# Kernel tuning notes

Hardware: AMD Instinct MI355X
Metric: run time of the kernel (lower is better)

## Reference

```python
import jax, jax.numpy as jnp
import numpy as np

N = 50000      # nodes
E = 400000     # edges
F_IN = 64      # raw node feat
E_IN = 16      # raw edge feat
H = 128        # hidden
L = 4          # PNAConv layers
G = 256        # graphs in batch
OUT = 12       # classes
EPS = 1e-5


def setup_inputs() -> dict:
    key = jax.random.key(0)
    ks = jax.random.split(key, 24)
    s = 0.05
    inp = {
        'x': jax.random.normal(ks[0], (N, F_IN), jnp.float32),
        'edge_attr': jax.random.normal(ks[1], (E, E_IN), jnp.float32),
        'src': jax.random.randint(ks[2], (E,), 0, N, jnp.int32),
        'dst': jax.random.randint(ks[3], (E,), 0, N, jnp.int32),
        'batch': jnp.sort(jax.random.randint(ks[4], (N,), 0, G, jnp.int32)),
        'node_emb_W': jax.random.normal(ks[5], (F_IN, H), jnp.float32) * s,
        'node_emb_b': jnp.zeros((H,), jnp.float32),
        'edge_emb_W': jax.random.normal(ks[6], (E_IN, H), jnp.float32) * s,
        'edge_emb_b': jnp.zeros((H,), jnp.float32),
        'edge_enc_W': jax.random.normal(ks[7], (L, H, H), jnp.float32) * s,
        'edge_enc_b': jnp.zeros((L, H), jnp.float32),
        'pre_W': jax.random.normal(ks[8], (L, 3 * H, H), jnp.float32) * s,
        'pre_b': jnp.zeros((L, H), jnp.float32),
        'post_W': jax.random.normal(ks[9], (L, 13 * H, H), jnp.float32) * s,
        'post_b': jnp.zeros((L, H), jnp.float32),
        'lin_W': jax.random.normal(ks[10], (L, H, H), jnp.float32) * s,
        'lin_b': jnp.zeros((L, H), jnp.float32),
        'head_W': jax.random.normal(ks[11], (H, OUT), jnp.float32) * s,
        'head_b': jnp.zeros((OUT,), jnp.float32),
    }
    return inp


def pna_forward(x, edge_attr, src, dst, batch,
                node_emb_W, node_emb_b, edge_emb_W, edge_emb_b,
                edge_enc_W, edge_enc_b, pre_W, pre_b,
                post_W, post_b, lin_W, lin_b, head_W, head_b):
    n = x.shape[0]
    h = x @ node_emb_W + node_emb_b                     # [N,H]
    e0 = edge_attr @ edge_emb_W + edge_emb_b           # [E,H]

    ones = jnp.ones((src.shape[0],), jnp.float32)
    deg = jax.ops.segment_sum(ones, dst, num_segments=n)        # in-degree
    degc = jnp.maximum(deg, 1.0)                                 # PyG clamp_(1)
    avg_log = jnp.mean(jnp.log1p(deg))                           # avg_deg['log'] from histogram
    amp = (jnp.log(degc + 1.0) / avg_log)[:, None]               # amplification scaler
    att = (avg_log / jnp.log(degc + 1.0))[:, None]               # attenuation scaler
    has_nbr = (deg > 0)[:, None]

    for l in range(L):
        e = e0 @ edge_enc_W[l] + edge_enc_b[l]                   # [E,H]
        W = pre_W[l]
        # pre_nn(cat(x_i, x_j, e)) without materializing the 3H concat
        m = (jnp.take(h, dst, axis=0) @ W[:H] +
             jnp.take(h, src, axis=0) @ W[H:2 * H] +
             e @ W[2 * H:] + pre_b[l])                           # [E,H]
        s1 = jax.ops.segment_sum(m, dst, num_segments=n)
        mean = s1 / degc[:, None]
        mean2 = jax.ops.segment_sum(m * m, dst, num_segments=n) / degc[:, None]
        std = jnp.sqrt(jax.nn.relu(mean2 - mean * mean) + EPS)
        mn = jnp.where(has_nbr, jax.ops.segment_min(m, dst, num_segments=n), 0.0)
        mx = jnp.where(has_nbr, jax.ops.segment_max(m, dst, num_segments=n), 0.0)
        agg = jnp.concatenate([mean, mn, mx, std], axis=-1)      # [N,4H]
        scaled = jnp.concatenate([agg, agg * amp, agg * att], axis=-1)  # [N,12H]
        out = jnp.concatenate([h, scaled], axis=-1) @ post_W[l] + post_b[l]
        h = jax.nn.relu(out @ lin_W[l] + lin_b[l])               # dropout = identity (eval)

    g = jax.ops.segment_sum(h, batch, num_segments=G)            # global_add_pool
    return g @ head_W + head_b                                   # [G,12]


def reference(x, edge_attr, src, dst, batch,
              node_emb_W, node_emb_b, edge_emb_W, edge_emb_b,
              edge_enc_W, edge_enc_b, pre_W, pre_b,
              post_W, post_b, lin_W, lin_b, head_W, head_b):
    return pna_forward(x, edge_attr, src, dst, batch,
                       node_emb_W, node_emb_b, edge_emb_W, edge_emb_b,
                       edge_enc_W, edge_enc_b, pre_W, pre_b,
                       post_W, post_b, lin_W, lin_b, head_W, head_b)
```

## Files before the change

### kernel.cpp

```cpp
#include <hip/hip_runtime.h>

#define NN 50000
#define NE 400000
#define FIN 64
#define EIN 16
#define H 128
#define NL 4
#define NG 256
#define NOUT 12
#define EPSV 1e-5f

#define SB 256
#define NBLK ((NN + SB - 1) / SB)
#define GB2 ((NN + 127) / 128)
#define NP64 (NN * 64)

typedef short bf16x8 __attribute__((ext_vector_type(8)));
typedef float f32x4 __attribute__((ext_vector_type(4)));
typedef float v2f __attribute__((ext_vector_type(2)));

__device__ __forceinline__ unsigned short f2bf(float f) {
    unsigned u = __float_as_uint(f);
    u += 0x7fffu + ((u >> 16) & 1u);
    return (unsigned short)(u >> 16);
}

__device__ __forceinline__ float bflo(unsigned u) { return __uint_as_float(u << 16); }
__device__ __forceinline__ float bfhi(unsigned u) { return __uint_as_float(u & 0xffff0000u); }

__global__ void k_hist(const int* __restrict__ dst, int* __restrict__ deg) {
    int e = blockIdx.x * 256 + threadIdx.x;
    if (e < NE) atomicAdd(&deg[dst[e]], 1);
}

__global__ void k_scan1(const int* __restrict__ deg, int* __restrict__ partial) {
    __shared__ int sm[256];
    int i = blockIdx.x * 256 + threadIdx.x;
    sm[threadIdx.x] = (i < NN) ? deg[i] : 0;
    __syncthreads();
    for (int s = 128; s > 0; s >>= 1) {
        if (threadIdx.x < s) sm[threadIdx.x] += sm[threadIdx.x + s];
        __syncthreads();
    }
    if (threadIdx.x == 0) partial[blockIdx.x] = sm[0];
}

__global__ void k_scan2(int* __restrict__ partial, int* __restrict__ row_ptr, int nblk) {
    __shared__ int sm[256];
    int t = threadIdx.x;
    sm[t] = (t < nblk) ? partial[t] : 0;
    __syncthreads();
    for (int off = 1; off < 256; off <<= 1) {
        int v = (t >= off) ? sm[t - off] : 0;
        __syncthreads();
        sm[t] += v;
        __syncthreads();
    }
    int excl = (t == 0) ? 0 : sm[t - 1];
    if (t < nblk) partial[t] = excl;
    if (t == 0) row_ptr[0] = 0;
}

__global__ void k_scan3(const int* __restrict__ deg, const int* __restrict__ partial,
                        int* __restrict__ row_ptr) {
    __shared__ int sm[256];
    int t = threadIdx.x;
    int i = blockIdx.x * 256 + t;
    sm[t] = (i < NN) ? deg[i] : 0;
    __syncthreads();
    for (int off = 1; off < 256; off <<= 1) {
        int v = (t >= off) ? sm[t - off] : 0;
        __syncthreads();
        sm[t] += v;
        __syncthreads();
    }
    if (i < NN) row_ptr[i + 1] = partial[blockIdx.x] + sm[t];
}

__global__ void k_fill(const int* __restrict__ src, const int* __restrict__ dst,
                       const int* __restrict__ row_ptr, int* __restrict__ cursor,
                       int* __restrict__ csr_src, int* __restrict__ csr_eid) {
    int e = blockIdx.x * 256 + threadIdx.x;
    if (e >= NE) return;
    int d = dst[e];
    int pos = atomicAdd(&cursor[d], 1);
    int slot = row_ptr[d] + pos;
    csr_src[slot] = src[e];
    csr_eid[slot] = e;
}

__global__ void k_eperm(const float* __restrict__ eattr, const int* __restrict__ csr_eid,
                        float* __restrict__ eattrF) {
    int idx = blockIdx.x * 256 + threadIdx.x;
    if (idx >= NE * EIN) return;
    int slot = idx >> 4, j = idx & 15;
    eattrF[idx] = eattr[(size_t)csr_eid[slot] * EIN + j];
}

__global__ void k_sumlog(const int* __restrict__ deg, float* __restrict__ sum) {
    int i = blockIdx.x * 256 + threadIdx.x;
    float v = (i < NN) ? log1pf((float)deg[i]) : 0.f;
    #pragma unroll
    for (int off = 32; off > 0; off >>= 1) v += __shfl_down(v, off, 64);
    if ((threadIdx.x & 63) == 0) atomicAdd(sum, v);
}

__global__ void k_scalers(const int* __restrict__ deg, const float* __restrict__ sumlog,
                          float* __restrict__ amp, float* __restrict__ att) {
    int i = blockIdx.x * 256 + threadIdx.x;
    if (i >= NN) return;
    float avg = sumlog[0] / (float)NN;
    float degc = fmaxf((float)deg[i], 1.0f);
    float la = logf(degc + 1.0f);
    amp[i] = la / avg;
    att[i] = avg / la;
}

__global__ __launch_bounds__(256) void k_encfold(const float* __restrict__ encW,
                                                 const float* __restrict__ preW,
                                                 float* __restrict__ M) {
    __shared__ float As[32][68];
    __shared__ float Bs[32][128];
    int l = blockIdx.y;
    const float* A = encW + (size_t)l * H * H;
    const float* Bp = preW + (size_t)l * 3 * H * H + 2 * H * H;
    float* Ml = M + (size_t)l * H * H;
    int m0 = blockIdx.x * 64;
    int tid = threadIdx.x;
    int tx = tid & 31, ty = tid >> 5;
    float4 acc[8];
    #pragma unroll
    for (int r = 0; r < 8; r++) acc[r] = make_float4(0, 0, 0, 0);
    int f = tid & 7, r0 = tid >> 3;
    int cf = tid & 31, kr0 = tid >> 5;
    for (int k0 = 0; k0 < H; k0 += 32) {
        #pragma unroll
        for (int hh = 0; hh < 2; hh++) {
            int r = r0 + hh * 32;
            float4 v = *(const float4*)(A + (size_t)(m0 + r) * H + k0 + f * 4);
            As[f * 4 + 0][r] = v.x; As[f * 4 + 1][r] = v.y;
            As[f * 4 + 2][r] = v.z; As[f * 4 + 3][r] = v.w;
        }
        #pragma unroll
        for (int hh = 0; hh < 4; hh++) {
            int kr = kr0 + hh * 8;
            *(float4*)&Bs[kr][cf * 4] = *(const float4*)(Bp + (size_t)(k0 + kr) * H + cf * 4);
        }
        __syncthreads();
        #pragma unroll
        for (int kk = 0; kk < 32; kk++) {
            float4 b = *(float4*)&Bs[kk][tx * 4];
            float4 a0 = *(float4*)&As[kk][ty * 8];
            float4 a1 = *(float4*)&As[kk][ty * 8 + 4];
            acc[0].x = fmaf(a0.x, b.x, acc[0].x); acc[0].y = fmaf(a0.x, b.y, acc[0].y);
            acc[0].z = fmaf(a0.x, b.z, acc[0].z); acc[0].w = fmaf(a0.x, b.w, acc[0].w);
            acc[1].x = fmaf(a0.y, b.x, acc[1].x); acc[1].y = fmaf(a0.y, b.y, acc[1].y);
            acc[1].z = fmaf(a0.y, b.z, acc[1].z); acc[1].w = fmaf(a0.y, b.w, acc[1].w);
            acc[2].x = fmaf(a0.z, b.x, acc[2].x); acc[2].y = fmaf(a0.z, b.y, acc[2].y);
            acc[2].z = fmaf(a0.z, b.z, acc[2].z); acc[2].w = fmaf(a0.z, b.w, acc[2].w);
            acc[3].x = fmaf(a0.w, b.x, acc[3].x); acc[3].y = fmaf(a0.w, b.y, acc[3].y);
            acc[3].z = fmaf(a0.w, b.z, acc[3].z); acc[3].w = fmaf(a0.w, b.w, acc[3].w);
            acc[4].x = fmaf(a1.x, b.x, acc[4].x); acc[4].y = fmaf(a1.x, b.y, acc[4].y);
            acc[4].z = fmaf(a1.x, b.z, acc[4].z); acc[4].w = fmaf(a1.x, b.w, acc[4].w);
            acc[5].x = fmaf(a1.y, b.x, acc[5].x); acc[5].y = fmaf(a1.y, b.y, acc[5].y);
            acc[5].z = fmaf(a1.y, b.z, acc[5].z); acc[5].w = fmaf(a1.y, b.w, acc[5].w);
            acc[6].x = fmaf(a1.z, b.x, acc[6].x); acc[6].y = fmaf(a1.z, b.y, acc[6].y);
            acc[6].z = fmaf(a1.z, b.z, acc[6].z); acc[6].w = fmaf(a1.z, b.w, acc[6].w);
            acc[7].x = fmaf(a1.w, b.x, acc[7].x); acc[7].y = fmaf(a1.w, b.y, acc[7].y);
            acc[7].z = fmaf(a1.w, b.z, acc[7].z); acc[7].w = fmaf(a1.w, b.w, acc[7].w);
        }
        __syncthreads();
    }
    #pragma unroll
    for (int rr = 0; rr < 8; rr++) {
        int row = m0 + ty * 8 + rr;
        *(float4*)(Ml + (size_t)row * H + tx * 4) = acc[rr];
    }
}

__global__ void k_kprep(const float* __restrict__ embW, const float* __restrict__ M,
                        float* __restrict__ Kc) {
    int l = blockIdx.y;
    int idx = blockIdx.x * 256 + threadIdx.x;
    int r = idx >> 7, j = idx & 127;
    const float* Ml = M + (size_t)l * H * H;
    float s = 0.f;
    for (int k = 0; k < H; k++) s = fmaf(embW[r * H + k], Ml[k * H + j], s);
    Kc[l * 16 * H + idx] = s;
}

__global__ void k_cprep(const float* __restrict__ emb_b, const float* __restrict__ encW,
                        const float* __restrict__ enc_b, const float* __restrict__ preW,
                        const float* __restrict__ pre_b, float* __restrict__ cc) {
    __shared__ float b1[H];
    int l = blockIdx.x, t = threadIdx.x;
    const float* encWl = encW + (size_t)l * H * H;
    const float* preW2 = preW + (size_t)l * 3 * H * H + 2 * H * H;
    float s = enc_b[l * H + t];
    for (int k = 0; k < H; k++) s = fmaf(emb_b[k], encWl[k * H + t], s);
    b1[t] = s;
    __syncthreads();
    float c = pre_b[l * H + t];
    for (int k = 0; k < H; k++) c = fmaf(b1[k], preW2[k * H + t], c);
    cc[l * H + t] = c;
}

struct TD { const float* S; unsigned short* D; int K; };
struct TDs { TD t[9]; };

__global__ void k_prepw(TDs p) {
    TD d = p.t[blockIdx.y];
    int idx = blockIdx.x * 256 + threadIdx.x;
    int total = d.K << 7;
    if (idx < total) {
        int k = idx >> 7, n = idx & 127;
        d.D[(size_t)n * d.K + k] = f2bf(d.S[(size_t)k * 128 + n]);
    }
}

__global__ void k_cast(const float* __restrict__ S, unsigned short* __restrict__ D, int n) {
    int i = blockIdx.x * 256 + threadIdx.x;
    if (i < n) D[i] = f2bf(S[i]);
}

__global__ __launch_bounds__(256) void k_wfold(const float* __restrict__ postW,
                                               const float* __restrict__ linW,
                                               unsigned short* __restrict__ Wt3,
                                               unsigned short* __restrict__ foldT) {
    __shared__ float As[32][68];
    __shared__ float Bs[32][128];
    int l = blockIdx.y;
    const float* A = postW + (size_t)l * 13 * H * H;
    const float* Bp = linW + (size_t)l * H * H;
    int m0 = blockIdx.x * 64;
    int tid = threadIdx.x;
    int tx = tid & 31, ty = tid >> 5;
    float4 acc[8];
    #pragma unroll
    for (int r = 0; r < 8; r++) acc[r] = make_float4(0, 0, 0, 0);
    int f = tid & 7, r0 = tid >> 3;
    int cf = tid & 31, kr0 = tid >> 5;
    for (int k0 = 0; k0 < H; k0 += 32) {
        #pragma unroll
        for (int hh = 0; hh < 2; hh++) {
            int r = r0 + hh * 32;
            float4 v = *(const float4*)(A + (size_t)(m0 + r) * H + k0 + f * 4);
            As[f * 4 + 0][r] = v.x; As[f * 4 + 1][r] = v.y;
            As[f * 4 + 2][r] = v.z; As[f * 4 + 3][r] = v.w;
        }
        #pragma unroll
        for (int hh = 0; hh < 4; hh++) {
            int kr = kr0 + hh * 8;
            *(float4*)&Bs[kr][cf * 4] = *(const float4*)(Bp + (size_t)(k0 + kr) * H + cf * 4);
        }
        __syncthreads();
        #pragma unroll
        for (int kk = 0; kk < 32; kk++) {
            float4 b = *(float4*)&Bs[kk][tx * 4];
            float4 a0 = *(float4*)&As[kk][ty * 8];
            float4 a1 = *(float4*)&As[kk][ty * 8 + 4];
            acc[0].x = fmaf(a0.x, b.x, acc[0].x); acc[0].y = fmaf(a0.x, b.y, acc[0].y);
            acc[0].z = fmaf(a0.x, b.z, acc[0].z); acc[0].w = fmaf(a0.x, b.w, acc[0].w);
            acc[1].x = fmaf(a0.y, b.x, acc[1].x); acc[1].y = fmaf(a0.y, b.y, acc[1].y);
            acc[1].z = fmaf(a0.y, b.z, acc[1].z); acc[1].w = fmaf(a0.y, b.w, acc[1].w);
            acc[2].x = fmaf(a0.z, b.x, acc[2].x); acc[2].y = fmaf(a0.z, b.y, acc[2].y);
            acc[2].z = fmaf(a0.z, b.z, acc[2].z); acc[2].w = fmaf(a0.z, b.w, acc[2].w);
            acc[3].x = fmaf(a0.w, b.x, acc[3].x); acc[3].y = fmaf(a0.w, b.y, acc[3].y);
            acc[3].z = fmaf(a0.w, b.z, acc[3].z); acc[3].w = fmaf(a0.w, b.w, acc[3].w);
            acc[4].x = fmaf(a1.x, b.x, acc[4].x); acc[4].y = fmaf(a1.x, b.y, acc[4].y);
            acc[4].z = fmaf(a1.x, b.z, acc[4].z); acc[4].w = fmaf(a1.x, b.w, acc[4].w);
            acc[5].x = fmaf(a1.y, b.x, acc[5].x); acc[5].y = fmaf(a1.y, b.y, acc[5].y);
            acc[5].z = fmaf(a1.y, b.z, acc[5].z); acc[5].w = fmaf(a1.y, b.w, acc[5].w);
            acc[6].x = fmaf(a1.z, b.x, acc[6].x); acc[6].y = fmaf(a1.z, b.y, acc[6].y);
            acc[6].z = fmaf(a1.z, b.z, acc[6].z); acc[6].w = fmaf(a1.z, b.w, acc[6].w);
            acc[7].x = fmaf(a1.w, b.x, acc[7].x); acc[7].y = fmaf(a1.w, b.y, acc[7].y);
            acc[7].z = fmaf(a1.w, b.z, acc[7].z); acc[7].w = fmaf(a1.w, b.w, acc[7].w);
        }
        __syncthreads();
    }
    unsigned short* w2 = Wt3 + (size_t)(l * 3 + 2) * H * H;
    unsigned short* ft = foldT + (size_t)l * 128 * 1664;
    int r = m0 + ty * 8;
    #pragma unroll
    for (int c = 0; c < 4; c++) {
        int n = tx * 4 + c;
        unsigned short tmp[8] __attribute__((aligned(16)));
        #pragma unroll
        for (int rr = 0; rr < 8; rr++) tmp[rr] = f2bf(((const float*)&acc[rr])[c]);
        unsigned short* dstp = (r < 128) ? (w2 + (size_t)n * 128 + r)
                                         : (ft + (size_t)n * 1664 + r);
        *(uint4*)dstp = *(const uint4*)tmp;
    }
}

__global__ void k_bfold(const float* __restrict__ pb, const float* __restrict__ lb,
                        const float* __restrict__ linW, float* __restrict__ cf) {
    int l = blockIdx.x, n = threadIdx.x;
    const float* B = linW + (size_t)l * H * H;
    float s = lb[l * H + n];
    for (int j = 0; j < H; j++) s = fmaf(pb[l * H + j], B[j * H + n], s);
    cf[l * H + n] = s;
}

__global__ __launch_bounds__(256, 4) void k_mgemm(
    const unsigned short* __restrict__ A, int lda, int K, int nch,
    const unsigned short* __restrict__ Bt, int ldb, int bstride_y,
    const float* __restrict__ bias, unsigned short* __restrict__ outB)
{
    __shared__ unsigned short SH[2][128][72];
    const unsigned short* Btp = Bt + (size_t)blockIdx.x * bstride_y;
    int m0 = blockIdx.y * 128;
    int tid = threadIdx.x;
    int wave = tid >> 6, lane = tid & 63;
    int wr = wave >> 1, wc = wave & 1;
    int ln = lane & 15, q = lane >> 4;

    f32x4 acc[4][4];
    #pragma unroll
    for (int a = 0; a < 4; a++)
        #pragma unroll
        for (int b = 0; b < 4; b++) acc[a][b] = (f32x4){0.f, 0.f, 0.f, 0.f};

    for (int c = 0; c < nch; c++) {
        int col = c * 64;
        #pragma unroll
        for (int i0 = 0; i0 < 4; i0++) {
            int i = tid + i0 * 256;
            int row = i >> 3, seg = i & 7;
            uint4 bv = *(const uint4*)(Btp + (size_t)row * ldb + col + seg * 8);
            *(uint4*)(&SH[1][row][seg * 8]) = bv;
            int rowg = m0 + row;
            uint4 av = make_uint4(0, 0, 0, 0);
            if (rowg < NN) av = *(const uint4*)(A + (size_t)rowg * lda + col + seg * 8);
            *(uint4*)(&SH[0][row][seg * 8]) = av;
        }
        __syncthreads();
        #pragma unroll
        for (int kq = 0; kq < 2; kq++) {
            bf16x8 af[4], bfr[4];
            #pragma unroll
            for (int f = 0; f < 4; f++) {
                af[f]  = *(const bf16x8*)(&SH[0][wr * 64 + f * 16 + ln][kq * 32 + q * 8]);
                bfr[f] = *(const bf16x8*)(&SH[1][wc * 64 + f * 16 + ln][kq * 32 + q * 8]);
            }
            #pragma unroll
            for (int fr = 0; fr < 4; fr++)
                #pragma unroll
                for (int fc = 0; fc < 4; fc++)
                    acc[fr][fc] = __builtin_amdgcn_mfma_f32_16x16x32_bf16(
                        bfr[fc], af[fr], acc[fr][fc], 0, 0, 0);
        }
        __syncthreads();
    }

    unsigned short* CT = &SH[0][0][0];
    #pragma unroll
    for (int fr = 0; fr < 4; fr++) {
        int rloc = wr * 64 + fr * 16 + ln;
        #pragma unroll
        for (int fc = 0; fc < 4; fc++) {
            int colb = wc * 64 + fc * 16 + q * 4;
            float4 bv = bias ? *(const float4*)(bias + colb) : make_float4(0, 0, 0, 0);
            unsigned short tmp[4] __attribute__((aligned(8)));
            tmp[0] = f2bf(acc[fr][fc][0] + bv.x);
            tmp[1] = f2bf(acc[fr][fc][1] + bv.y);
            tmp[2] = f2bf(acc[fr][fc][2] + bv.z);
            tmp[3] = f2bf(acc[fr][fc][3] + bv.w);
            *(uint2*)(&CT[rloc * 136 + colb]) = *(const uint2*)tmp;
        }
    }
    __syncthreads();
    unsigned short* outBp = outB + (size_t)blockIdx.x * NN * H;
    #pragma unroll
    for (int i0 = 0; i0 < 8; i0++) {
        int idx = tid + i0 * 256;
        int row = idx >> 4, seg = idx & 15;
        int rowg = m0 + row;
        if (rowg < NN)
            *(uint4*)(outBp + (size_t)rowg * H + seg * 8) = *(const uint4*)(&CT[row * 136 + seg * 8]);
    }
}

__global__ __launch_bounds__(256) void k_agg2(
    const unsigned short* __restrict__ pd, const unsigned short* __restrict__ ps,
    const float* __restrict__ eF,
    const int* __restrict__ csr_src, const int* __restrict__ row_ptr,
    const float* __restrict__ Kl, const float* __restrict__ cl,
    unsigned short* __restrict__ agg)
{
    int wv = threadIdx.x >> 6, lane = threadIdx.x & 63;
    int i = blockIdx.x * 4 + wv;
    int d0 = lane * 2;
    v2f kr[16];
    #pragma unroll
    for (int k = 0; k < 16; k++) kr[k] = *(const v2f*)(Kl + k * H + d0);
    v2f c2 = *(const v2f*)(cl + d0);
    unsigned hd = *(const unsigned*)(pd + (size_t)i * H + d0);
    v2f base = c2 + (v2f){bflo(hd), bfhi(hd)};
    int rs = __builtin_amdgcn_readfirstlane(row_ptr[i]);
    int re = __builtin_amdgcn_readfirstlane(row_ptr[i + 1]);
    v2f s = (v2f){0.f, 0.f}, qv = (v2f){0.f, 0.f};
    v2f mn = (v2f){3.0e38f, 3.0e38f}, mx = (v2f){-3.0e38f, -3.0e38f};

    unsigned hs0, hs1, hs2, hs3;
    {
        int a0 = (rs < re)     ? __builtin_amdgcn_readfirstlane(csr_src[rs])     : 0;
        int a1 = (rs + 1 < re) ? __builtin_amdgcn_readfirstlane(csr_src[rs + 1]) : 0;
        int a2 = (rs + 2 < re) ? __builtin_amdgcn_readfirstlane(csr_src[rs + 2]) : 0;
        int a3 = (rs + 3 < re) ? __builtin_amdgcn_readfirstlane(csr_src[rs + 3]) : 0;
        hs0 = *(const unsigned*)(ps + (size_t)a0 * H + d0);
        hs1 = *(const unsigned*)(ps + (size_t)a1 * H + d0);
        hs2 = *(const unsigned*)(ps + (size_t)a2 * H + d0);
        hs3 = *(const unsigned*)(ps + (size_t)a3 * H + d0);
    }

    int slot = rs;
    for (; slot + 1 < re; slot += 2) {
        int p0 = (slot + 4 < re) ? __builtin_amdgcn_readfirstlane(csr_src[slot + 4]) : 0;
        int p1 = (slot + 5 < re) ? __builtin_amdgcn_readfirstlane(csr_src[slot + 5]) : 0;
        unsigned hsN0 = *(const unsigned*)(ps + (size_t)p0 * H + d0);
        unsigned hsN1 = *(const unsigned*)(ps + (size_t)p1 * H + d0);
        const float* ea = eF + (size_t)slot * EIN;
        const float* eb = ea + EIN;
        v2f a = base + (v2f){bflo(hs0), bfhi(hs0)};
        v2f c = base + (v2f){bflo(hs1), bfhi(hs1)};
        #pragma unroll
        for (int j = 0; j < 16; j++) {
            float e1 = ea[j], e2 = eb[j];
            a = (v2f){e1, e1} * kr[j] + a;
            c = (v2f){e2, e2} * kr[j] + c;
        }
        s = s + a + c;
        qv = a * a + (c * c + qv);
        mn.x = fminf(mn.x, fminf(a.x, c.x)); mn.y = fminf(mn.y, fminf(a.y, c.y));
        mx.x = fmaxf(mx.x, fmaxf(a.x, c.x)); mx.y = fmaxf(mx.y, fmaxf(a.y, c.y));
        hs0 = hs2; hs1 = hs3; hs2 = hsN0; hs3 = hsN1;
    }
    if (slot < re) {
        const float* ea = eF + (size_t)slot * EIN;
        v2f a = base + (v2f){bflo(hs0), bfhi(hs0)};
        #pragma unroll
        for (int j = 0; j < 16; j++) {
            float e1 = ea[j];
            a = (v2f){e1, e1} * kr[j] + a;
        }
        s = s + a;
        qv = a * a + qv;
        mn.x = fminf(mn.x, a.x); mn.y = fminf(mn.y, a.y);
        mx.x = fmaxf(mx.x, a.x); mx.y = fmaxf(mx.y, a.y);
    }

    int dg = re - rs;
    float dinv = 1.0f / fmaxf((float)dg, 1.0f);
    v2f me = s * (v2f){dinv, dinv};
    float sdx = sqrtf(fmaxf(qv.x * dinv - me.x * me.x, 0.f) + EPSV);
    float sdy = sqrtf(fmaxf(qv.y * dinv - me.y * me.y, 0.f) + EPSV);
    if (dg == 0) { mn = (v2f){0.f, 0.f}; mx = (v2f){0.f, 0.f}; }
    unsigned short* ap = agg + (size_t)i * 512 + d0;
    *(unsigned*)(ap)       = (unsigned)f2bf(me.x) | ((unsigned)f2bf(me.y) << 16);
    *(unsigned*)(ap + 128) = (unsigned)f2bf(mn.x) | ((unsigned)f2bf(mn.y) << 16);
    *(unsigned*)(ap + 256) = (unsigned)f2bf(mx.x) | ((unsigned)f2bf(mx.y) << 16);
    *(unsigned*)(ap + 384) = (unsigned)f2bf(sdx)  | ((unsigned)f2bf(sdy)  << 16);
}

__global__ __launch_bounds__(256) void k_comb(const unsigned* __restrict__ ha,
                                              const unsigned* __restrict__ part,
                                              const float* __restrict__ amp,
                                              const float* __restrict__ att,
                                              const float* __restrict__ biasf,
                                              unsigned* __restrict__ hbo,
                                              float* __restrict__ hfo) {
    int dv = blockIdx.x * 256 + threadIdx.x;
    int i = dv >> 6;
    int cp = dv & 63;
    float a = amp[i], t = att[i];
    unsigned uh = ha[dv];
    unsigned p0 = part[dv];
    unsigned p1 = part[dv + NP64];
    unsigned p2 = part[dv + 2 * NP64];
    float lo = bflo(uh) + bflo(p0) + a * bflo(p1) + t * bflo(p2) + biasf[cp * 2];
    float hi = bfhi(uh) + bfhi(p0) + a * bfhi(p1) + t * bfhi(p2) + biasf[cp * 2 + 1];
    lo = fmaxf(lo, 0.f); hi = fmaxf(hi, 0.f);
    hbo[dv] = (unsigned)f2bf(lo) | ((unsigned)f2bf(hi) << 16);
    if (hfo) { hfo[dv * 2] = lo; hfo[dv * 2 + 1] = hi; }
}

__device__ __forceinline__ int lbound(const int* a, int n, int v) {
    int lo = 0, hi = n;
    while (lo < hi) { int m = (lo + hi) >> 1; if (a[m] < v) lo = m + 1; else hi = m; }
    return lo;
}

__global__ __launch_bounds__(256) void k_pool(const float* __restrict__ h,
                                              const int* __restrict__ batch,
                                              const float* __restrict__ headW,
                                              const float* __restrict__ headb,
                                              float* __restrict__ out) {
    __shared__ float sm[256];
    int g = blockIdx.x;
    int t = threadIdx.x;
    int col = t & 127;
    int half = t >> 7;
    int lo = lbound(batch, NN, g);
    int hi = lbound(batch, NN, g + 1);
    int mid = lo + ((hi - lo) >> 1);
    int b0 = half ? mid : lo;
    int b1 = half ? hi : mid;
    float acc = 0.f;
    for (int i = b0; i < b1; i++) acc += h[(size_t)i * H + col];
    sm[t] = acc;
    __syncthreads();
    if (t < 128) sm[t] += sm[t + 128];
    __syncthreads();
    if (t < NOUT) {
        float r = headb[t];
        for (int j = 0; j < H; j++) r = fmaf(sm[j], headW[j * NOUT + t], r);
        out[g * NOUT + t] = r;
    }
}

extern "C" void kernel_launch(void* const* d_in, const int* in_sizes, int n_in,
                              void* d_out, int out_size, void* d_ws, size_t ws_size,
                              hipStream_t stream) {
    const float* x          = (const float*)d_in[0];
    const float* edge_attr  = (const float*)d_in[1];
    const int*   src        = (const int*)d_in[2];
    const int*   dst        = (const int*)d_in[3];
    const int*   batch      = (const int*)d_in[4];
    const float* node_emb_W = (const float*)d_in[5];
    const float* node_emb_b = (const float*)d_in[6];
    const float* edge_emb_W = (const float*)d_in[7];
    const float* edge_emb_b = (const float*)d_in[8];
    const float* edge_enc_W = (const float*)d_in[9];
    const float* edge_enc_b = (const float*)d_in[10];
    const float* pre_W      = (const float*)d_in[11];
    const float* pre_b      = (const float*)d_in[12];
    const float* post_W     = (const float*)d_in[13];
    const float* post_b     = (const float*)d_in[14];
    const float* lin_W      = (const float*)d_in[15];
    const float* lin_b      = (const float*)d_in[16];
    const float* head_W     = (const float*)d_in[17];
    const float* head_b     = (const float*)d_in[18];
    float* out = (float*)d_out;

    char* wp = (char*)d_ws;
    auto carve = [&](size_t bytes) -> char* {
        char* r = wp;
        wp += (bytes + 255) & ~(size_t)255;
        return r;
    };
    int*   deg     = (int*)carve((size_t)NN * 4);
    int*   cursor  = (int*)carve((size_t)NN * 4);
    float* sumlog  = (float*)carve(4);
    int*   partial = (int*)carve(256 * 4);
    int*   row_ptr = (int*)carve((size_t)(NN + 1) * 4);
    int*   csr_src = (int*)carve((size_t)NE * 4);
    int*   csr_eid = (int*)carve((size_t)NE * 4);
    float* amp     = (float*)carve((size_t)NN * 4);
    float* att     = (float*)carve((size_t)NN * 4);
    float* Kc      = (float*)carve((size_t)NL * 16 * H * 4);
    float* cc      = (float*)carve((size_t)NL * H * 4);
    float* cfold   = (float*)carve((size_t)NL * H * 4);
    float* Mf      = (float*)carve((size_t)NL * H * H * 4);
    float* eattrF  = (float*)carve((size_t)NE * EIN * 4);
    unsigned short* embWt  = (unsigned short*)carve((size_t)H * FIN * 2);
    unsigned short* Wt3    = (unsigned short*)carve((size_t)NL * 3 * H * H * 2);
    unsigned short* foldT  = (unsigned short*)carve((size_t)NL * 128 * 1664 * 2);
    unsigned short* xb     = (unsigned short*)carve((size_t)NN * FIN * 2);
    unsigned short* hb     = (unsigned short*)carve((size_t)NN * H * 2);
    unsigned short* planesB= (unsigned short*)carve((size_t)3 * NN * H * 2);
    unsigned short* aggb   = (unsigned short*)carve((size_t)NN * 4 * H * 2);
    unsigned short* partsB = (unsigned short*)carve((size_t)3 * NN * H * 2);
    float* hf      = (float*)carve((size_t)NN * H * 4);

    const size_t NP = (size_t)NN * H;

    hipMemsetAsync(deg, 0, ((size_t)NN * 4 + 255 & ~(size_t)255) * 2 + 256, stream);

    k_hist<<<(NE + 255) / 256, 256, 0, stream>>>(dst, deg);
    k_scan1<<<NBLK, 256, 0, stream>>>(deg, partial);
    k_scan2<<<1, 256, 0, stream>>>(partial, row_ptr, NBLK);
    k_scan3<<<NBLK, 256, 0, stream>>>(deg, partial, row_ptr);
    k_fill<<<(NE + 255) / 256, 256, 0, stream>>>(src, dst, row_ptr, cursor, csr_src, csr_eid);
    k_eperm<<<(NE * EIN + 255) / 256, 256, 0, stream>>>(edge_attr, csr_eid, eattrF);
    k_sumlog<<<NBLK, 256, 0, stream>>>(deg, sumlog);
    k_scalers<<<NBLK, 256, 0, stream>>>(deg, sumlog, amp, att);
    k_encfold<<<dim3(2, NL), 256, 0, stream>>>(edge_enc_W, pre_W, Mf);
    k_kprep<<<dim3(8, NL), 256, 0, stream>>>(edge_emb_W, Mf, Kc);
    k_cprep<<<NL, H, 0, stream>>>(edge_emb_b, edge_enc_W, edge_enc_b, pre_W, pre_b, cc);
    k_wfold<<<dim3(26, NL), 256, 0, stream>>>(post_W, lin_W, Wt3, foldT);
    k_bfold<<<NL, H, 0, stream>>>(post_b, lin_b, lin_W, cfold);

    TDs tds;
    int nd = 0;
    tds.t[nd++] = TD{node_emb_W, embWt, FIN};
    for (int l = 0; l < NL; l++) {
        tds.t[nd++] = TD{pre_W + (size_t)l * 3 * H * H,         Wt3 + (size_t)(l * 3 + 0) * H * H, H};
        tds.t[nd++] = TD{pre_W + (size_t)l * 3 * H * H + H * H, Wt3 + (size_t)(l * 3 + 1) * H * H, H};
    }
    k_prepw<<<dim3(64, 9), 256, 0, stream>>>(tds);
    k_cast<<<(NN * FIN + 255) / 256, 256, 0, stream>>>(x, xb, NN * FIN);

    k_mgemm<<<dim3(1, GB2), 256, 0, stream>>>(xb, FIN, FIN, 1, embWt, FIN, 0,
                                              node_emb_b, hb);

    for (int l = 0; l < NL; l++) {
        int last = (l == NL - 1);
        k_mgemm<<<dim3(3, GB2), 256, 0, stream>>>(hb, H, H, 2,
                                                  Wt3 + (size_t)l * 3 * H * H, H, H * H,
                                                  nullptr, planesB);
        k_agg2<<<NN / 4, 256, 0, stream>>>(planesB, planesB + NP,
                                           eattrF, csr_src, row_ptr,
                                           Kc + (size_t)l * 16 * H, cc + (size_t)l * H,
                                           aggb);
        k_mgemm<<<dim3(3, GB2), 256, 0, stream>>>(aggb, 4 * H, 4 * H, 8,
                                                  foldT + (size_t)l * 128 * 1664 + 128,
                                                  1664, 512,
                                                  nullptr, partsB);
        k_comb<<<NP64 / 256, 256, 0, stream>>>((const unsigned*)(planesB + 2 * NP),
                                               (const unsigned*)partsB, amp, att,
                                               cfold + (size_t)l * H,
                                               (unsigned*)hb, last ? hf : nullptr);
    }

    k_pool<<<NG, 256, 0, stream>>>(hf, batch, head_W, head_b, out);
}
```

Baseline: 778.5 us.

## Fuse post-aggregation GEMM with scaler combine epilogue; prefetch edge features in agg

```diff
diff --git a/kernel.cpp b/kernel.cpp
--- a/kernel.cpp
+++ b/kernel.cpp
@@ -13,6 +13,7 @@
 #define SB 256
 #define NBLK ((NN + SB - 1) / SB)
 #define GB2 ((NN + 127) / 128)
+#define GB3 ((NN + 63) / 64)
 #define NP64 (NN * 64)
 
 typedef short bf16x8 __attribute__((ext_vector_type(8)));
@@ -381,6 +382,128 @@
     }
 }
 
+__global__ __launch_bounds__(256, 3) void k_pgemm(
+    const unsigned short* __restrict__ A,
+    const unsigned short* __restrict__ Bt,
+    const unsigned short* __restrict__ ha,
+    const float* __restrict__ amp, const float* __restrict__ att,
+    const float* __restrict__ biasf,
+    unsigned short* __restrict__ outB, float* __restrict__ outF)
+{
+    __shared__ unsigned short SH[64 * 72 + 128 * 72];
+    unsigned short (*As)[72] = (unsigned short(*)[72])SH;
+    unsigned short (*Bs)[72] = (unsigned short(*)[72])(SH + 64 * 72);
+    int m0 = blockIdx.x * 64;
+    int tid = threadIdx.x;
+    int wave = tid >> 6, lane = tid & 63;
+    int wr = wave >> 1, wc = wave & 1;
+    int ln = lane & 15, q = lane >> 4;
+
+    float sc1[2], sc2[2];
+    #pragma unroll
+    for (int fr = 0; fr < 2; fr++) {
+        int row = m0 + wr * 32 + fr * 16 + ln;
+        row = row < NN ? row : NN - 1;
+        sc1[fr] = amp[row];
+        sc2[fr] = att[row];
+    }
+
+    f32x4 tot[2][4];
+    #pragma unroll
+    for (int a = 0; a < 2; a++)
+        #pragma unroll
+        for (int b = 0; b < 4; b++) tot[a][b] = (f32x4){0.f, 0.f, 0.f, 0.f};
+
+    for (int g = 0; g < 3; g++) {
+        f32x4 acc[2][4];
+        #pragma unroll
+        for (int a = 0; a < 2; a++)
+            #pragma unroll
+            for (int b = 0; b < 4; b++) acc[a][b] = (f32x4){0.f, 0.f, 0.f, 0.f};
+
+        for (int c = 0; c < 8; c++) {
+            int kofs = 128 + g * 512 + c * 64;
+            #pragma unroll
+            for (int i0 = 0; i0 < 2; i0++) {
+                int i = tid + i0 * 256;
+                int row = i >> 3, seg = i & 7;
+                int rowg = m0 + row;
+                uint4 av = make_uint4(0, 0, 0, 0);
+                if (rowg < NN) av = *(const uint4*)(A + (size_t)rowg * 512 + c * 64 + seg * 8);
+                *(uint4*)(&As[row][seg * 8]) = av;
+            }
+            #pragma unroll
+            for (int i0 = 0; i0 < 4; i0++) {
+                int i = tid + i0 * 256;
+                int n = i >> 3, seg = i & 7;
+                uint4 bv = *(const uint4*)(Bt + (size_t)n * 1664 + kofs + seg * 8);
+                *(uint4*)(&Bs[n][seg * 8]) = bv;
+            }
+            __syncthreads();
+            #pragma unroll
+            for (int kq = 0; kq < 2; kq++) {
+                bf16x8 af[2], bfr[4];
+                #pragma unroll
+                for (int f = 0; f < 2; f++)
+                    af[f] = *(const bf16x8*)(&As[wr * 32 + f * 16 + ln][kq * 32 + q * 8]);
+                #pragma unroll
+                for (int f = 0; f < 4; f++)
+                    bfr[f] = *(const bf16x8*)(&Bs[wc * 64 + f * 16 + ln][kq * 32 + q * 8]);
+                #pragma unroll
+                for (int fr = 0; fr < 2; fr++)
+                    #pragma unroll
+                    for (int fc = 0; fc < 4; fc++)
+                        acc[fr][fc] = __builtin_amdgcn_mfma_f32_16x16x32_bf16(
+                            bfr[fc], af[fr], acc[fr][fc], 0, 0, 0);
+            }
+            __syncthreads();
+        }
+        #pragma unroll
+        for (int fr = 0; fr < 2; fr++) {
+            float s = (g == 0) ? 1.0f : (g == 1 ? sc1[fr] : sc2[fr]);
+            #pragma unroll
+            for (int fc = 0; fc < 4; fc++) {
+                tot[fr][fc][0] = fmaf(s, acc[fr][fc][0], tot[fr][fc][0]);
+                tot[fr][fc][1] = fmaf(s, acc[fr][fc][1], tot[fr][fc][1]);
+                tot[fr][fc][2] = fmaf(s, acc[fr][fc][2], tot[fr][fc][2]);
+                tot[fr][fc][3] = fmaf(s, acc[fr][fc][3], tot[fr][fc][3]);
+            }
+        }
+    }
+
+    unsigned short* CT = SH;
+    #pragma unroll
+    for (int fr = 0; fr < 2; fr++) {
+        int rloc = wr * 32 + fr * 16 + ln;
+        int row = m0 + rloc;
+        int rc = row < NN ? row : NN - 1;
+        #pragma unroll
+        for (int fc = 0; fc < 4; fc++) {
+            int colb = wc * 64 + fc * 16 + q * 4;
+            float4 bv = *(const float4*)(biasf + colb);
+            uint2 h2 = *(const uint2*)(ha + (size_t)rc * H + colb);
+            float v0 = fmaxf(tot[fr][fc][0] + bflo(h2.x) + bv.x, 0.f);
+            float v1 = fmaxf(tot[fr][fc][1] + bfhi(h2.x) + bv.y, 0.f);
+            float v2 = fmaxf(tot[fr][fc][2] + bflo(h2.y) + bv.z, 0.f);
+            float v3 = fmaxf(tot[fr][fc][3] + bfhi(h2.y) + bv.w, 0.f);
+            unsigned short tmp[4] __attribute__((aligned(8)));
+            tmp[0] = f2bf(v0); tmp[1] = f2bf(v1); tmp[2] = f2bf(v2); tmp[3] = f2bf(v3);
+            *(uint2*)(&CT[rloc * 136 + colb]) = *(const uint2*)tmp;
+            if (outF && row < NN)
+                *(float4*)(outF + (size_t)row * H + colb) = make_float4(v0, v1, v2, v3);
+        }
+    }
+    __syncthreads();
+    #pragma unroll
+    for (int i0 = 0; i0 < 4; i0++) {
+        int idx = tid + i0 * 256;
+        int row = idx >> 4, seg = idx & 15;
+        int rowg = m0 + row;
+        if (rowg < NN)
+            *(uint4*)(outB + (size_t)rowg * H + seg * 8) = *(const uint4*)(&CT[row * 136 + seg * 8]);
+    }
+}
+
 __global__ __launch_bounds__(256) void k_agg2(
     const unsigned short* __restrict__ pd, const unsigned short* __restrict__ ps,
     const float* __restrict__ eF,
@@ -403,6 +526,7 @@
     v2f mn = (v2f){3.0e38f, 3.0e38f}, mx = (v2f){-3.0e38f, -3.0e38f};
 
     unsigned hs0, hs1, hs2, hs3;
+    float4 eA[4], eB[4];
     {
         int a0 = (rs < re)     ? __builtin_amdgcn_readfirstlane(csr_src[rs])     : 0;
         int a1 = (rs + 1 < re) ? __builtin_amdgcn_readfirstlane(csr_src[rs + 1]) : 0;
@@ -412,16 +536,30 @@
         hs1 = *(const unsigned*)(ps + (size_t)a1 * H + d0);
         hs2 = *(const unsigned*)(ps + (size_t)a2 * H + d0);
         hs3 = *(const unsigned*)(ps + (size_t)a3 * H + d0);
+        int s0 = (rs < re) ? rs : 0;
+        int s1 = (rs + 1 < re) ? rs + 1 : s0;
+        const float4* p0 = (const float4*)(eF + (size_t)s0 * EIN);
+        const float4* p1 = (const float4*)(eF + (size_t)s1 * EIN);
+        #pragma unroll
+        for (int w = 0; w < 4; w++) { eA[w] = p0[w]; eB[w] = p1[w]; }
     }
 
     int slot = rs;
     for (; slot + 1 < re; slot += 2) {
-        int p0 = (slot + 4 < re) ? __builtin_amdgcn_readfirstlane(csr_src[slot + 4]) : 0;
-        int p1 = (slot + 5 < re) ? __builtin_amdgcn_readfirstlane(csr_src[slot + 5]) : 0;
-        unsigned hsN0 = *(const unsigned*)(ps + (size_t)p0 * H + d0);
-        unsigned hsN1 = *(const unsigned*)(ps + (size_t)p1 * H + d0);
-        const float* ea = eF + (size_t)slot * EIN;
-        const float* eb = ea + EIN;
+        int p0i = (slot + 4 < re) ? __builtin_amdgcn_readfirstlane(csr_src[slot + 4]) : 0;
+        int p1i = (slot + 5 < re) ? __builtin_amdgcn_readfirstlane(csr_src[slot + 5]) : 0;
+        unsigned hsN0 = *(const unsigned*)(ps + (size_t)p0i * H + d0);
+        unsigned hsN1 = *(const unsigned*)(ps + (size_t)p1i * H + d0);
+        int s2 = (slot + 2 < re) ? slot + 2 : slot;
+        int s3 = (slot + 3 < re) ? slot + 3 : slot;
+        const float4* pn0 = (const float4*)(eF + (size_t)s2 * EIN);
+        const float4* pn1 = (const float4*)(eF + (size_t)s3 * EIN);
+        float4 nA[4], nB[4];
+        #pragma unroll
+        for (int w = 0; w < 4; w++) { nA[w] = pn0[w]; nB[w] = pn1[w]; }
+
+        const float* ea = (const float*)eA;
+        const float* eb = (const float*)eB;
         v2f a = base + (v2f){bflo(hs0), bfhi(hs0)};
         v2f c = base + (v2f){bflo(hs1), bfhi(hs1)};
         #pragma unroll
@@ -435,9 +573,11 @@
         mn.x = fminf(mn.x, fminf(a.x, c.x)); mn.y = fminf(mn.y, fminf(a.y, c.y));
         mx.x = fmaxf(mx.x, fmaxf(a.x, c.x)); mx.y = fmaxf(mx.y, fmaxf(a.y, c.y));
         hs0 = hs2; hs1 = hs3; hs2 = hsN0; hs3 = hsN1;
+        #pragma unroll
+        for (int w = 0; w < 4; w++) { eA[w] = nA[w]; eB[w] = nB[w]; }
     }
     if (slot < re) {
-        const float* ea = eF + (size_t)slot * EIN;
+        const float* ea = (const float*)eA;
         v2f a = base + (v2f){bflo(hs0), bfhi(hs0)};
         #pragma unroll
         for (int j = 0; j < 16; j++) {
@@ -461,28 +601,6 @@
     *(unsigned*)(ap + 128) = (unsigned)f2bf(mn.x) | ((unsigned)f2bf(mn.y) << 16);
     *(unsigned*)(ap + 256) = (unsigned)f2bf(mx.x) | ((unsigned)f2bf(mx.y) << 16);
     *(unsigned*)(ap + 384) = (unsigned)f2bf(sdx)  | ((unsigned)f2bf(sdy)  << 16);
-}
-
-__global__ __launch_bounds__(256) void k_comb(const unsigned* __restrict__ ha,
-                                              const unsigned* __restrict__ part,
-                                              const float* __restrict__ amp,
-                                              const float* __restrict__ att,
-                                              const float* __restrict__ biasf,
-                                              unsigned* __restrict__ hbo,
-                                              float* __restrict__ hfo) {
-    int dv = blockIdx.x * 256 + threadIdx.x;
-    int i = dv >> 6;
-    int cp = dv & 63;
-    float a = amp[i], t = att[i];
-    unsigned uh = ha[dv];
-    unsigned p0 = part[dv];
-    unsigned p1 = part[dv + NP64];
-    unsigned p2 = part[dv + 2 * NP64];
-    float lo = bflo(uh) + bflo(p0) + a * bflo(p1) + t * bflo(p2) + biasf[cp * 2];
-    float hi = bfhi(uh) + bfhi(p0) + a * bfhi(p1) + t * bfhi(p2) + biasf[cp * 2 + 1];
-    lo = fmaxf(lo, 0.f); hi = fmaxf(hi, 0.f);
-    hbo[dv] = (unsigned)f2bf(lo) | ((unsigned)f2bf(hi) << 16);
-    if (hfo) { hfo[dv * 2] = lo; hfo[dv * 2 + 1] = hi; }
 }
 
 __device__ __forceinline__ int lbound(const int* a, int n, int v) {
@@ -570,7 +688,6 @@
     unsigned short* hb     = (unsigned short*)carve((size_t)NN * H * 2);
     unsigned short* planesB= (unsigned short*)carve((size_t)3 * NN * H * 2);
     unsigned short* aggb   = (unsigned short*)carve((size_t)NN * 4 * H * 2);
-    unsigned short* partsB = (unsigned short*)carve((size_t)3 * NN * H * 2);
     float* hf      = (float*)carve((size_t)NN * H * 4);
 
     const size_t NP = (size_t)NN * H;
@@ -613,14 +730,10 @@
                                            eattrF, csr_src, row_ptr,
                                            Kc + (size_t)l * 16 * H, cc + (size_t)l * H,
                                            aggb);
-        k_mgemm<<<dim3(3, GB2), 256, 0, stream>>>(aggb, 4 * H, 4 * H, 8,
-                                                  foldT + (size_t)l * 128 * 1664 + 128,
-                                                  1664, 512,
-                                                  nullptr, partsB);
-        k_comb<<<NP64 / 256, 256, 0, stream>>>((const unsigned*)(planesB + 2 * NP),
-                                               (const unsigned*)partsB, amp, att,
-                                               cfold + (size_t)l * H,
-                                               (unsigned*)hb, last ? hf : nullptr);
+        k_pgemm<<<GB3, 256, 0, stream>>>(aggb, foldT + (size_t)l * 128 * 1664,
+                                         planesB + 2 * NP, amp, att,
+                                         cfold + (size_t)l * H,
+                                         hb, last ? hf : nullptr);
     }
 
     k_pool<<<NG, 256, 0, stream>>>(hf, batch, head_W, head_b, out);
```

Result: slower. 876.4 us (+12.6%).

## Split each node's edge list across two waves and prefetch edge features

Applied to the files above, without the earlier changes.

```diff
diff --git a/kernel.cpp b/kernel.cpp
--- a/kernel.cpp
+++ b/kernel.cpp
@@ -388,8 +388,10 @@
     const float* __restrict__ Kl, const float* __restrict__ cl,
     unsigned short* __restrict__ agg)
 {
+    __shared__ float smf[4][64][8];
     int wv = threadIdx.x >> 6, lane = threadIdx.x & 63;
-    int i = blockIdx.x * 4 + wv;
+    int i = blockIdx.x * 2 + (wv >> 1);
+    int half = wv & 1;
     int d0 = lane * 2;
     v2f kr[16];
     #pragma unroll
@@ -397,12 +399,16 @@
     v2f c2 = *(const v2f*)(cl + d0);
     unsigned hd = *(const unsigned*)(pd + (size_t)i * H + d0);
     v2f base = c2 + (v2f){bflo(hd), bfhi(hd)};
-    int rs = __builtin_amdgcn_readfirstlane(row_ptr[i]);
-    int re = __builtin_amdgcn_readfirstlane(row_ptr[i + 1]);
+    int rsN = __builtin_amdgcn_readfirstlane(row_ptr[i]);
+    int reN = __builtin_amdgcn_readfirstlane(row_ptr[i + 1]);
+    int mid = rsN + ((reN - rsN + 1) >> 1);
+    int rs = half ? mid : rsN;
+    int re = half ? reN : mid;
     v2f s = (v2f){0.f, 0.f}, qv = (v2f){0.f, 0.f};
     v2f mn = (v2f){3.0e38f, 3.0e38f}, mx = (v2f){-3.0e38f, -3.0e38f};
 
     unsigned hs0, hs1, hs2, hs3;
+    float4 eA[4], eB[4];
     {
         int a0 = (rs < re)     ? __builtin_amdgcn_readfirstlane(csr_src[rs])     : 0;
         int a1 = (rs + 1 < re) ? __builtin_amdgcn_readfirstlane(csr_src[rs + 1]) : 0;
@@ -412,16 +418,30 @@
         hs1 = *(const unsigned*)(ps + (size_t)a1 * H + d0);
         hs2 = *(const unsigned*)(ps + (size_t)a2 * H + d0);
         hs3 = *(const unsigned*)(ps + (size_t)a3 * H + d0);
+        int s0 = (rs < re) ? rs : 0;
+        int s1 = (rs + 1 < re) ? rs + 1 : s0;
+        const float4* p0 = (const float4*)(eF + (size_t)s0 * EIN);
+        const float4* p1 = (const float4*)(eF + (size_t)s1 * EIN);
+        #pragma unroll
+        for (int w = 0; w < 4; w++) { eA[w] = p0[w]; eB[w] = p1[w]; }
     }
 
     int slot = rs;
     for (; slot + 1 < re; slot += 2) {
-        int p0 = (slot + 4 < re) ? __builtin_amdgcn_readfirstlane(csr_src[slot + 4]) : 0;
-        int p1 = (slot + 5 < re) ? __builtin_amdgcn_readfirstlane(csr_src[slot + 5]) : 0;
-        unsigned hsN0 = *(const unsigned*)(ps + (size_t)p0 * H + d0);
-        unsigned hsN1 = *(const unsigned*)(ps + (size_t)p1 * H + d0);
-        const float* ea = eF + (size_t)slot * EIN;
-        const float* eb = ea + EIN;
+        int p0i = (slot + 4 < re) ? __builtin_amdgcn_readfirstlane(csr_src[slot + 4]) : 0;
+        int p1i = (slot + 5 < re) ? __builtin_amdgcn_readfirstlane(csr_src[slot + 5]) : 0;
+        unsigned hsN0 = *(const unsigned*)(ps + (size_t)p0i * H + d0);
+        unsigned hsN1 = *(const unsigned*)(ps + (size_t)p1i * H + d0);
+        int s2 = (slot + 2 < re) ? slot + 2 : slot;
+        int s3 = (slot + 3 < re) ? slot + 3 : slot;
+        const float4* pn0 = (const float4*)(eF + (size_t)s2 * EIN);
+        const float4* pn1 = (const float4*)(eF + (size_t)s3 * EIN);
+        float4 nA[4], nB[4];
+        #pragma unroll
+        for (int w = 0; w < 4; w++) { nA[w] = pn0[w]; nB[w] = pn1[w]; }
+
+        const float* ea = (const float*)eA;
+        const float* eb = (const float*)eB;
         v2f a = base + (v2f){bflo(hs0), bfhi(hs0)};
         v2f c = base + (v2f){bflo(hs1), bfhi(hs1)};
         #pragma unroll
@@ -435,9 +455,11 @@
         mn.x = fminf(mn.x, fminf(a.x, c.x)); mn.y = fminf(mn.y, fminf(a.y, c.y));
         mx.x = fmaxf(mx.x, fmaxf(a.x, c.x)); mx.y = fmaxf(mx.y, fmaxf(a.y, c.y));
         hs0 = hs2; hs1 = hs3; hs2 = hsN0; hs3 = hsN1;
+        #pragma unroll
+        for (int w = 0; w < 4; w++) { eA[w] = nA[w]; eB[w] = nB[w]; }
     }
     if (slot < re) {
-        const float* ea = eF + (size_t)slot * EIN;
+        const float* ea = (const float*)eA;
         v2f a = base + (v2f){bflo(hs0), bfhi(hs0)};
         #pragma unroll
         for (int j = 0; j < 16; j++) {
@@ -450,7 +472,18 @@
         mx.x = fmaxf(mx.x, a.x); mx.y = fmaxf(mx.y, a.y);
     }
 
-    int dg = re - rs;
+    float* sw = smf[wv][lane];
+    sw[0] = s.x; sw[1] = s.y; sw[2] = qv.x; sw[3] = qv.y;
+    sw[4] = mn.x; sw[5] = mn.y; sw[6] = mx.x; sw[7] = mx.y;
+    __syncthreads();
+    if (half) return;
+    const float* po = smf[wv + 1][lane];
+    s.x += po[0]; s.y += po[1];
+    qv.x += po[2]; qv.y += po[3];
+    mn.x = fminf(mn.x, po[4]); mn.y = fminf(mn.y, po[5]);
+    mx.x = fmaxf(mx.x, po[6]); mx.y = fmaxf(mx.y, po[7]);
+
+    int dg = reN - rsN;
     float dinv = 1.0f / fmaxf((float)dg, 1.0f);
     v2f me = s * (v2f){dinv, dinv};
     float sdx = sqrtf(fmaxf(qv.x * dinv - me.x * me.x, 0.f) + EPSV);
@@ -609,7 +642,7 @@
         k_mgemm<<<dim3(3, GB2), 256, 0, stream>>>(hb, H, H, 2,
                                                   Wt3 + (size_t)l * 3 * H * H, H, H * H,
                                                   nullptr, planesB);
-        k_agg2<<<NN / 4, 256, 0, stream>>>(planesB, planesB + NP,
+        k_agg2<<<NN / 2, 256, 0, stream>>>(planesB, planesB + NP,
                                            eattrF, csr_src, row_ptr,
                                            Kc + (size_t)l * 16 * H, cc + (size_t)l * H,
                                            aggb);
```

New measurement: 1.250 ms. +60.6%, slower.
